# Performance work log

Hardware: AMD Instinct MI355X
Metric: run time of the kernel (lower is better)

Reference implementation:

```python
import jax, jax.numpy as jnp
import numpy as np

N, F, D, K, H, O = 100000, 128, 16, 8, 256, 256  # nodes, feat, degree, num_hash, hash_dim, out_dim


def setup_inputs() -> dict:
    key = jax.random.key(0)
    k1, k2, k3, k4, k5 = jax.random.split(key, 5)
    x = jax.random.normal(k1, (N, F), dtype=jnp.float32)
    nbr_idx = jax.random.randint(k2, (N, D), 0, N, dtype=jnp.int32)
    # fixed sign hash matrices, one per hasher: {+1,-1}^{F x H}
    R = (jax.random.uniform(k3, (K, F, H)) > 0.5).astype(jnp.float32) * 2.0 - 1.0
    lim = float(np.sqrt(6.0 / (K * H + O)))  # xavier_uniform for Linear(K*H, O)
    Ws = jax.random.uniform(k4, (O, K * H), jnp.float32, -lim, lim)
    Wn = jax.random.uniform(k5, (O, K * H), jnp.float32, -lim, lim)
    bias = jnp.zeros((O,), dtype=jnp.float32)
    return {"x": x, "nbr_idx": nbr_idx, "R": R, "Ws": Ws, "Wn": Wn, "bias": bias}


def reference(x, nbr_idx, R, Ws, Wn, bias):
    n, f = x.shape
    k, _, h = R.shape
    # gather neighbor feats [N, D, F] and degree-mean -> [N, F]
    # (hashing is linear, so mean(hash(neigh)) == hash(mean(neigh)))
    neigh_mean = jnp.mean(x[nbr_idx], axis=1)
    # hash with all K hashers and concatenate streams: [N, K*H]
    hashed_neigh = jnp.einsum('nf,kfh->nkh', neigh_mean, R).reshape(n, k * h)
    hashed_self = jnp.einsum('nf,kfh->nkh', x, R).reshape(n, k * h)
    out = hashed_neigh @ Wn.T + hashed_self @ Ws.T + bias
    return jax.nn.elu(out)
```

## Files before the change

kernel.cpp:

```cpp
#include <hip/hip_runtime.h>
#include <hip/hip_bf16.h>
#include <math.h>

#define NN 100000
#define FF 128
#define DD 16
#define KK 8
#define HH 256
#define OO 256
#define KH 2048

using frag_t  = __attribute__((ext_vector_type(8))) short;
using f32x4   = __attribute__((ext_vector_type(4))) float;
using ushort8 = __attribute__((ext_vector_type(8))) unsigned short;

static __device__ __forceinline__ float bf2f(unsigned int u16) {
    union { unsigned int i; float f; } v; v.i = u16 << 16; return v.f;
}
static __device__ __forceinline__ float blo(unsigned int u) {
    union { unsigned int i; float f; } v; v.i = u << 16; return v.f;
}
static __device__ __forceinline__ float bhi(unsigned int u) {
    union { unsigned int i; float f; } v; v.i = u & 0xffff0000u; return v.f;
}
static __device__ __forceinline__ unsigned short f2bf(float f) {
    union { float f; unsigned int i; } v; v.f = f;
    unsigned int x = v.i;
    x += 0x7fffu + ((x >> 16) & 1u);
    return (unsigned short)(x >> 16);
}

__global__ __launch_bounds__(256) void k_cast(const float* __restrict__ x,
                                              unsigned short* __restrict__ xb) {
    int t = blockIdx.x * 256 + threadIdx.x;
    const float4* xv = (const float4*)x;
    float4 a = xv[2 * t], b = xv[2 * t + 1];
    ushort8 o;
    o[0] = f2bf(a.x); o[1] = f2bf(a.y); o[2] = f2bf(a.z); o[3] = f2bf(a.w);
    o[4] = f2bf(b.x); o[5] = f2bf(b.y); o[6] = f2bf(b.z); o[7] = f2bf(b.w);
    *(ushort8*)(xb + (size_t)t * 8) = o;
}

__global__ __launch_bounds__(256) void k_wgemm(const float* __restrict__ R,
                                               const float* __restrict__ Ws,
                                               const float* __restrict__ Wn,
                                               float* __restrict__ P) {
    __shared__ float a_s[16][68];
    __shared__ float w_s[16][68];
    int bx = blockIdx.x, by = blockIdx.y, bz = blockIdx.z;
    const float* W = (bx < 2) ? Wn : Ws;
    int fbase = (bx & 1) * 64;
    int t = threadIdx.x;
    int tx = t & 15, ty = t >> 4;
    int lf = t >> 2;
    int j4 = (t & 3) * 4;
    float acc[4][4] = {};
    const float* Rb = R + (size_t)bz * (FF * HH) + (size_t)(fbase + lf) * HH;
    const float* Wb = W + (size_t)(by * 64 + lf) * KH + (size_t)bz * 256;
    for (int ks = 0; ks < 16; ++ks) {
        float4 av = *(const float4*)(Rb + ks * 16 + j4);
        float4 wv = *(const float4*)(Wb + ks * 16 + j4);
        __syncthreads();
        a_s[j4 + 0][lf] = av.x; a_s[j4 + 1][lf] = av.y;
        a_s[j4 + 2][lf] = av.z; a_s[j4 + 3][lf] = av.w;
        w_s[j4 + 0][lf] = wv.x; w_s[j4 + 1][lf] = wv.y;
        w_s[j4 + 2][lf] = wv.z; w_s[j4 + 3][lf] = wv.w;
        __syncthreads();
#pragma unroll
        for (int jj = 0; jj < 16; ++jj) {
            float ar[4], wr[4];
#pragma unroll
            for (int i = 0; i < 4; ++i) ar[i] = a_s[jj][ty * 4 + i];
#pragma unroll
            for (int j = 0; j < 4; ++j) wr[j] = w_s[jj][tx * 4 + j];
#pragma unroll
            for (int i = 0; i < 4; ++i)
#pragma unroll
                for (int j = 0; j < 4; ++j) acc[i][j] += ar[i] * wr[j];
        }
    }
    float* Pb = P + (size_t)bz * 65536 + (size_t)(bx * 64) * 256 + by * 64;
#pragma unroll
    for (int i = 0; i < 4; ++i) {
        float4 v = make_float4(acc[i][0], acc[i][1], acc[i][2], acc[i][3]);
        *(float4*)(Pb + (size_t)(ty * 4 + i) * 256 + tx * 4) = v;
    }
}

__global__ __launch_bounds__(256) void k_comb(const float* __restrict__ P,
                                              unsigned short* __restrict__ Bbf) {
    __shared__ float tsh[64][65];
    int bf = blockIdx.x, bo = blockIdx.y;
    int t = threadIdx.x;
    for (int e = t; e < 4096; e += 256) {
        int r = e >> 6, c = e & 63;
        float s = 0.f;
#pragma unroll
        for (int z = 0; z < 8; ++z)
            s += P[(size_t)z * 65536 + (size_t)(bf * 64 + r) * 256 + bo * 64 + c];
        tsh[r][c] = s;
    }
    __syncthreads();
    for (int e = t; e < 4096; e += 256) {
        int r = e >> 6, c = e & 63;
        Bbf[(size_t)(bo * 64 + r) * 256 + bf * 64 + c] = f2bf(tsh[c][r]);
    }
}

__global__ __launch_bounds__(512, 4) void k_fused(const unsigned short* __restrict__ xb,
                                                  const int* __restrict__ nbr,
                                                  const unsigned short* __restrict__ Bw,
                                                  const float* __restrict__ bias,
                                                  float* __restrict__ C) {
    __shared__ __align__(16) char smraw[64 * 264 * 2];
    unsigned short (*Als)[264] = (unsigned short (*)[264])smraw;
    float* Fls = (float*)smraw;
    const int FLS_W = 260;

    int m0 = blockIdx.x * 64;
    int t = threadIdx.x;
    int lane = t & 63, wv = t >> 6;
    int l15 = lane & 15, quad = lane >> 4;
    int l16 = lane & 15, r4 = lane >> 4;
    int selbase = (lane & 48) << 2;

#pragma unroll
    for (int g = 0; g < 2; ++g) {
        int row = wv * 8 + g * 4 + r4;
        int node = m0 + row; if (node >= NN) node = NN - 1;
        int myidx = nbr[(size_t)node * 16 + l16];
        uint4 selfv = *(const uint4*)(xb + (size_t)node * 128 + l16 * 8);
        float s[8] = {0.f, 0.f, 0.f, 0.f, 0.f, 0.f, 0.f, 0.f};
#pragma unroll
        for (int h = 0; h < 2; ++h) {
            uint4 gv[8];
#pragma unroll
            for (int d = 0; d < 8; ++d) {
                int bi = __builtin_amdgcn_ds_bpermute(selbase + ((h * 8 + d) << 2), myidx);
                gv[d] = *(const uint4*)(xb + (size_t)bi * 128 + l16 * 8);
            }
#pragma unroll
            for (int d = 0; d < 8; ++d) {
                s[0] += blo(gv[d].x); s[1] += bhi(gv[d].x);
                s[2] += blo(gv[d].y); s[3] += bhi(gv[d].y);
                s[4] += blo(gv[d].z); s[5] += bhi(gv[d].z);
                s[6] += blo(gv[d].w); s[7] += bhi(gv[d].w);
            }
        }
        ushort8 o;
#pragma unroll
        for (int k = 0; k < 8; ++k) o[k] = f2bf(s[k] * 0.0625f);
        *(ushort8*)&Als[row][l16 * 8] = o;
        *(uint4*)&Als[row][128 + l16 * 8] = selfv;
    }
    __syncthreads();

    f32x4 acc[4][2] = {};
#pragma unroll 1
    for (int kt = 0; kt < 4; ++kt) {
#pragma unroll
        for (int k2 = 0; k2 < 2; ++k2) {
            frag_t bfr[2], af[4];
#pragma unroll
            for (int j = 0; j < 2; ++j)
                bfr[j] = *(const frag_t*)(Bw + (size_t)(wv * 32 + j * 16 + l15) * 256
                                             + kt * 64 + k2 * 32 + quad * 8);
#pragma unroll
            for (int i = 0; i < 4; ++i)
                af[i] = *(const frag_t*)&Als[i * 16 + l15][kt * 64 + k2 * 32 + quad * 8];
#pragma unroll
            for (int i = 0; i < 4; ++i)
#pragma unroll
                for (int j = 0; j < 2; ++j)
                    acc[i][j] = __builtin_amdgcn_mfma_f32_16x16x32_bf16(af[i], bfr[j], acc[i][j], 0, 0, 0);
        }
    }

    float bv[2];
#pragma unroll
    for (int j = 0; j < 2; ++j) bv[j] = bias[wv * 32 + j * 16 + l15];
#pragma unroll
    for (int p = 0; p < 2; ++p) {
        __syncthreads();
#pragma unroll
        for (int ii = 0; ii < 2; ++ii) {
            int i = p * 2 + ii;
#pragma unroll
            for (int j = 0; j < 2; ++j) {
                int col = wv * 32 + j * 16 + l15;
#pragma unroll
                for (int r = 0; r < 4; ++r) {
                    int lr = ii * 16 + quad * 4 + r;
                    float v = acc[i][j][r] + bv[j];
                    v = (v > 0.f) ? v : expm1f(v);
                    Fls[lr * FLS_W + col] = v;
                }
            }
        }
        __syncthreads();
#pragma unroll
        for (int q = 0; q < 4; ++q) {
            int f4 = q * 512 + t;
            int lr = f4 >> 6, c4 = f4 & 63;
            int grow = m0 + p * 32 + lr;
            if (grow < NN)
                *(float4*)(C + (size_t)grow * 256 + c4 * 4) = *(const float4*)&Fls[lr * FLS_W + c4 * 4];
        }
    }
}

extern "C" void kernel_launch(void* const* d_in, const int* in_sizes, int n_in,
                              void* d_out, int out_size, void* d_ws, size_t ws_size,
                              hipStream_t stream) {
    const float* x    = (const float*)d_in[0];
    const int*   nbr  = (const int*)d_in[1];
    const float* R    = (const float*)d_in[2];
    const float* Ws   = (const float*)d_in[3];
    const float* Wn   = (const float*)d_in[4];
    const float* bias = (const float*)d_in[5];
    float* out = (float*)d_out;

    char* ws = (char*)d_ws;
    unsigned short* xb  = (unsigned short*)(ws);
    float*          P   = (float*)(ws + 25600000);
    unsigned short* Bbf = (unsigned short*)(ws + 25600000 + 2097152);

    hipLaunchKernelGGL(k_cast,   dim3(6250),    dim3(256), 0, stream, x, xb);
    hipLaunchKernelGGL(k_wgemm,  dim3(4, 4, 8), dim3(256), 0, stream, R, Ws, Wn, P);
    hipLaunchKernelGGL(k_comb,   dim3(4, 4),    dim3(256), 0, stream, P, Bbf);
    hipLaunchKernelGGL(k_fused,  dim3(1563),    dim3(512), 0, stream, xb, nbr, Bbf, bias, out);
}
```

Before: 256.7 us.

## Merge cast and weight-projection GEMM into one MFMA prep kernel, batch gathers

Replaces the separate cast, fp32 split-K weight GEMM and combine kernels with a single prep kernel. Two blocks compute the folded R·W matrices with bf16 MFMA over the full K, while the remaining blocks cast x to bf16. The fused kernel now issues all 16 neighbour gathers at once, unrolls its k-loop by two, and uses __expf-1 for ELU. This removes two launches and the partial-sum buffer, at the cost of bf16 rounding of R and W inputs, higher register pressure, and a long serial GEMM on only two blocks.

```diff
diff --git a/kernel.cpp b/kernel.cpp
--- a/kernel.cpp
+++ b/kernel.cpp
@@ -14,9 +14,6 @@
 using f32x4   = __attribute__((ext_vector_type(4))) float;
 using ushort8 = __attribute__((ext_vector_type(8))) unsigned short;
 
-static __device__ __forceinline__ float bf2f(unsigned int u16) {
-    union { unsigned int i; float f; } v; v.i = u16 << 16; return v.f;
-}
 static __device__ __forceinline__ float blo(unsigned int u) {
     union { unsigned int i; float f; } v; v.i = u << 16; return v.f;
 }
@@ -29,81 +26,81 @@
     x += 0x7fffu + ((x >> 16) & 1u);
     return (unsigned short)(x >> 16);
 }
-
-__global__ __launch_bounds__(256) void k_cast(const float* __restrict__ x,
-                                              unsigned short* __restrict__ xb) {
-    int t = blockIdx.x * 256 + threadIdx.x;
-    const float4* xv = (const float4*)x;
-    float4 a = xv[2 * t], b = xv[2 * t + 1];
-    ushort8 o;
-    o[0] = f2bf(a.x); o[1] = f2bf(a.y); o[2] = f2bf(a.z); o[3] = f2bf(a.w);
-    o[4] = f2bf(b.x); o[5] = f2bf(b.y); o[6] = f2bf(b.z); o[7] = f2bf(b.w);
-    *(ushort8*)(xb + (size_t)t * 8) = o;
-}
-
-__global__ __launch_bounds__(256) void k_wgemm(const float* __restrict__ R,
-                                               const float* __restrict__ Ws,
-                                               const float* __restrict__ Wn,
-                                               float* __restrict__ P) {
-    __shared__ float a_s[16][68];
-    __shared__ float w_s[16][68];
-    int bx = blockIdx.x, by = blockIdx.y, bz = blockIdx.z;
-    const float* W = (bx < 2) ? Wn : Ws;
-    int fbase = (bx & 1) * 64;
+static __device__ __forceinline__ unsigned int pk2(float a, float b) {
+    return (unsigned int)f2bf(a) | ((unsigned int)f2bf(b) << 16);
+}
+
+__global__ __launch_bounds__(512) void k_prep(const float* __restrict__ x,
+                                              const float* __restrict__ R,
+                                              const float* __restrict__ Ws,
+                                              const float* __restrict__ Wn,
+                                              unsigned short* __restrict__ xb,
+                                              unsigned short* __restrict__ Bbf) {
+    __shared__ __align__(16) unsigned short Aw[256][72];
+    __shared__ __align__(16) unsigned short Bw[128][72];
+    int b = blockIdx.x;
     int t = threadIdx.x;
-    int tx = t & 15, ty = t >> 4;
-    int lf = t >> 2;
-    int j4 = (t & 3) * 4;
-    float acc[4][4] = {};
-    const float* Rb = R + (size_t)bz * (FF * HH) + (size_t)(fbase + lf) * HH;
-    const float* Wb = W + (size_t)(by * 64 + lf) * KH + (size_t)bz * 256;
-    for (int ks = 0; ks < 16; ++ks) {
-        float4 av = *(const float4*)(Rb + ks * 16 + j4);
-        float4 wv = *(const float4*)(Wb + ks * 16 + j4);
-        __syncthreads();
-        a_s[j4 + 0][lf] = av.x; a_s[j4 + 1][lf] = av.y;
-        a_s[j4 + 2][lf] = av.z; a_s[j4 + 3][lf] = av.w;
-        w_s[j4 + 0][lf] = wv.x; w_s[j4 + 1][lf] = wv.y;
-        w_s[j4 + 2][lf] = wv.z; w_s[j4 + 3][lf] = wv.w;
-        __syncthreads();
-#pragma unroll
-        for (int jj = 0; jj < 16; ++jj) {
-            float ar[4], wr[4];
-#pragma unroll
-            for (int i = 0; i < 4; ++i) ar[i] = a_s[jj][ty * 4 + i];
-#pragma unroll
-            for (int j = 0; j < 4; ++j) wr[j] = w_s[jj][tx * 4 + j];
-#pragma unroll
-            for (int i = 0; i < 4; ++i)
-#pragma unroll
-                for (int j = 0; j < 4; ++j) acc[i][j] += ar[i] * wr[j];
-        }
-    }
-    float* Pb = P + (size_t)bz * 65536 + (size_t)(bx * 64) * 256 + by * 64;
-#pragma unroll
-    for (int i = 0; i < 4; ++i) {
-        float4 v = make_float4(acc[i][0], acc[i][1], acc[i][2], acc[i][3]);
-        *(float4*)(Pb + (size_t)(ty * 4 + i) * 256 + tx * 4) = v;
-    }
-}
-
-__global__ __launch_bounds__(256) void k_comb(const float* __restrict__ P,
-                                              unsigned short* __restrict__ Bbf) {
-    __shared__ float tsh[64][65];
-    int bf = blockIdx.x, bo = blockIdx.y;
-    int t = threadIdx.x;
-    for (int e = t; e < 4096; e += 256) {
-        int r = e >> 6, c = e & 63;
-        float s = 0.f;
-#pragma unroll
-        for (int z = 0; z < 8; ++z)
-            s += P[(size_t)z * 65536 + (size_t)(bf * 64 + r) * 256 + bo * 64 + c];
-        tsh[r][c] = s;
-    }
-    __syncthreads();
-    for (int e = t; e < 4096; e += 256) {
-        int r = e >> 6, c = e & 63;
-        Bbf[(size_t)(bo * 64 + r) * 256 + bf * 64 + c] = f2bf(tsh[c][r]);
+    if (b >= 2) {
+        int g = (b - 2) * 512 + t;
+        const float4* xv = (const float4*)x;
+        float4 a = xv[2 * g], c = xv[2 * g + 1];
+        ushort8 o;
+        o[0] = f2bf(a.x); o[1] = f2bf(a.y); o[2] = f2bf(a.z); o[3] = f2bf(a.w);
+        o[4] = f2bf(c.x); o[5] = f2bf(c.y); o[6] = f2bf(c.z); o[7] = f2bf(c.w);
+        *(ushort8*)(xb + (size_t)g * 8) = o;
+        return;
+    }
+    const float* W = (b == 0) ? Wn : Ws;
+    int lane = t & 63, wv = t >> 6;
+    int wm = wv >> 1, wn = wv & 1;
+    int l15 = lane & 15, quad = lane >> 4;
+    f32x4 acc[4][4] = {};
+    for (int kt = 0; kt < 32; ++kt) {
+        __syncthreads();
+#pragma unroll
+        for (int s = 0; s < 8; ++s) {
+            int c = s * 512 + t;
+            int row = c >> 4, c4 = c & 15;
+            float4 v = *(const float4*)(W + (size_t)row * KH + kt * 64 + c4 * 4);
+            uint2 p; p.x = pk2(v.x, v.y); p.y = pk2(v.z, v.w);
+            *(uint2*)&Aw[row][c4 * 4] = p;
+        }
+#pragma unroll
+        for (int s = 0; s < 4; ++s) {
+            int c = s * 512 + t;
+            int row = c >> 4, c4 = c & 15;
+            float4 v = *(const float4*)(R + (size_t)(kt >> 2) * 32768
+                                          + (size_t)row * 256 + (kt & 3) * 64 + c4 * 4);
+            uint2 p; p.x = pk2(v.x, v.y); p.y = pk2(v.z, v.w);
+            *(uint2*)&Bw[row][c4 * 4] = p;
+        }
+        __syncthreads();
+#pragma unroll
+        for (int k2 = 0; k2 < 2; ++k2) {
+            frag_t af[4], bfr[4];
+#pragma unroll
+            for (int i = 0; i < 4; ++i)
+                af[i] = *(const frag_t*)&Aw[wm * 64 + i * 16 + l15][k2 * 32 + quad * 8];
+#pragma unroll
+            for (int j = 0; j < 4; ++j)
+                bfr[j] = *(const frag_t*)&Bw[wn * 64 + j * 16 + l15][k2 * 32 + quad * 8];
+#pragma unroll
+            for (int i = 0; i < 4; ++i)
+#pragma unroll
+                for (int j = 0; j < 4; ++j)
+                    acc[i][j] = __builtin_amdgcn_mfma_f32_16x16x32_bf16(af[i], bfr[j], acc[i][j], 0, 0, 0);
+        }
+    }
+#pragma unroll
+    for (int j = 0; j < 4; ++j) {
+        int f = wn * 64 + j * 16 + l15;
+#pragma unroll
+        for (int i = 0; i < 4; ++i) {
+            int o0 = wm * 64 + i * 16 + quad * 4;
+#pragma unroll
+            for (int r = 0; r < 4; ++r)
+                Bbf[(size_t)(o0 + r) * 256 + b * 128 + f] = f2bf(acc[i][j][r]);
+        }
     }
 }
 
@@ -130,22 +127,19 @@
         int node = m0 + row; if (node >= NN) node = NN - 1;
         int myidx = nbr[(size_t)node * 16 + l16];
         uint4 selfv = *(const uint4*)(xb + (size_t)node * 128 + l16 * 8);
+        uint4 gv[16];
+#pragma unroll
+        for (int d = 0; d < 16; ++d) {
+            int bi = __builtin_amdgcn_ds_bpermute(selbase + (d << 2), myidx);
+            gv[d] = *(const uint4*)(xb + (size_t)bi * 128 + l16 * 8);
+        }
         float s[8] = {0.f, 0.f, 0.f, 0.f, 0.f, 0.f, 0.f, 0.f};
 #pragma unroll
-        for (int h = 0; h < 2; ++h) {
-            uint4 gv[8];
-#pragma unroll
-            for (int d = 0; d < 8; ++d) {
-                int bi = __builtin_amdgcn_ds_bpermute(selbase + ((h * 8 + d) << 2), myidx);
-                gv[d] = *(const uint4*)(xb + (size_t)bi * 128 + l16 * 8);
-            }
-#pragma unroll
-            for (int d = 0; d < 8; ++d) {
-                s[0] += blo(gv[d].x); s[1] += bhi(gv[d].x);
-                s[2] += blo(gv[d].y); s[3] += bhi(gv[d].y);
-                s[4] += blo(gv[d].z); s[5] += bhi(gv[d].z);
-                s[6] += blo(gv[d].w); s[7] += bhi(gv[d].w);
-            }
+        for (int d = 0; d < 16; ++d) {
+            s[0] += blo(gv[d].x); s[1] += bhi(gv[d].x);
+            s[2] += blo(gv[d].y); s[3] += bhi(gv[d].y);
+            s[4] += blo(gv[d].z); s[5] += bhi(gv[d].z);
+            s[6] += blo(gv[d].w); s[7] += bhi(gv[d].w);
         }
         ushort8 o;
 #pragma unroll
@@ -156,7 +150,7 @@
     __syncthreads();
 
     f32x4 acc[4][2] = {};
-#pragma unroll 1
+#pragma unroll 2
     for (int kt = 0; kt < 4; ++kt) {
 #pragma unroll
         for (int k2 = 0; k2 < 2; ++k2) {
@@ -192,7 +186,7 @@
                 for (int r = 0; r < 4; ++r) {
                     int lr = ii * 16 + quad * 4 + r;
                     float v = acc[i][j][r] + bv[j];
-                    v = (v > 0.f) ? v : expm1f(v);
+                    v = (v > 0.f) ? v : (__expf(v) - 1.0f);
                     Fls[lr * FLS_W + col] = v;
                 }
             }
@@ -222,11 +216,8 @@
 
     char* ws = (char*)d_ws;
     unsigned short* xb  = (unsigned short*)(ws);
-    float*          P   = (float*)(ws + 25600000);
-    unsigned short* Bbf = (unsigned short*)(ws + 25600000 + 2097152);
-
-    hipLaunchKernelGGL(k_cast,   dim3(6250),    dim3(256), 0, stream, x, xb);
-    hipLaunchKernelGGL(k_wgemm,  dim3(4, 4, 8), dim3(256), 0, stream, R, Ws, Wn, P);
-    hipLaunchKernelGGL(k_comb,   dim3(4, 4),    dim3(256), 0, stream, P, Bbf);
-    hipLaunchKernelGGL(k_fused,  dim3(1563),    dim3(512), 0, stream, xb, nbr, Bbf, bias, out);
-}
+    unsigned short* Bbf = (unsigned short*)(ws + 25600000);
+
+    hipLaunchKernelGGL(k_prep,  dim3(3127), dim3(512), 0, stream, x, R, Ws, Wn, xb, Bbf);
+    hipLaunchKernelGGL(k_fused, dim3(1563), dim3(512), 0, stream, xb, nbr, Bbf, bias, out);
+}
```

Measured after the change: 329.2 us. 1.28x slower.
